# Performance work log

Hardware: AMD Instinct MI355X
Metric: run time of the kernel (lower is better)

## Reference

```python
import jax, jax.numpy as jnp
import numpy as np

D = 1024
H = 16
DK = D // H
E = 8
DFF = 4 * D
TOPK = 2
EPS = 1e-5


def setup_inputs() -> dict:
    key = jax.random.key(0)
    ks = jax.random.split(key, 16)
    s_in = 1.0 / np.sqrt(D)
    s_ff = 1.0 / np.sqrt(DFF)
    return {
        "x": jax.random.normal(ks[0], (2, 2048, D), dtype=jnp.float32),
        "ln1_g": jnp.ones((D,), jnp.float32),
        "ln1_b": jnp.zeros((D,), jnp.float32),
        "w_qkv": jax.random.normal(ks[1], (D, 3 * D), jnp.float32) * s_in,
        "b_qkv": jnp.zeros((3 * D,), jnp.float32),
        "w_o": jax.random.normal(ks[2], (D, D), jnp.float32) * s_in,
        "b_o": jnp.zeros((D,), jnp.float32),
        "ln2_g": jnp.ones((D,), jnp.float32),
        "ln2_b": jnp.zeros((D,), jnp.float32),
        "gate_w": jax.random.normal(ks[3], (D, E), jnp.float32) * s_in,
        "gate_b": jnp.zeros((E,), jnp.float32),
        "W1": jax.random.normal(ks[4], (E, D, DFF), jnp.float32) * s_in,
        "b1": jnp.zeros((E, DFF), jnp.float32),
        "W2": jax.random.normal(ks[5], (E, DFF, D), jnp.float32) * s_ff,
        "b2": jnp.zeros((E, D), jnp.float32),
    }


def _layernorm(x, g, b):
    m = jnp.mean(x, axis=-1, keepdims=True)
    v = jnp.mean(jnp.square(x - m), axis=-1, keepdims=True)
    return (x - m) * jax.lax.rsqrt(v + EPS) * g + b


def reference(x, ln1_g, ln1_b, w_qkv, b_qkv, w_o, b_o, ln2_g, ln2_b,
              gate_w, gate_b, W1, b1, W2, b2):
    B, S, _ = x.shape
    # --- attention (pre-LN, residual) ---
    h = _layernorm(x, ln1_g, ln1_b)
    qkv = h @ w_qkv + b_qkv                      # [B,S,3D]
    q, k, v = jnp.split(qkv, 3, axis=-1)
    q = q.reshape(B, S, H, DK)
    k = k.reshape(B, S, H, DK)
    v = v.reshape(B, S, H, DK)
    scores = jnp.einsum('bqhd,bkhd->bhqk', q, k) / np.sqrt(DK)
    attn = jax.nn.softmax(scores, axis=-1)
    o = jnp.einsum('bhqk,bkhd->bqhd', attn, v).reshape(B, S, D)
    x = x + o @ w_o + b_o
    # --- MoE (pre-LN, residual) ---
    h = _layernorm(x, ln2_g, ln2_b).reshape(B * S, D)   # [T,D]
    logits = h @ gate_w + gate_b                        # [T,E]
    topv, topi = jax.lax.top_k(logits, TOPK)            # [T,K]
    gw = jax.nn.softmax(topv, axis=-1)                  # [T,K]
    # per-token per-expert combine weight (0 if expert not selected)
    ew = jnp.sum(jax.nn.one_hot(topi, E, dtype=h.dtype) * gw[..., None], axis=1)  # [T,E]
    hid = jax.nn.relu(jnp.einsum('td,edf->etf', h, W1) + b1[:, None, :])  # [E,T,DFF]
    out_e = jnp.einsum('etf,efd->etd', hid, W2) + b2[:, None, :]          # [E,T,D]
    moe = jnp.einsum('etd,te->td', out_e, ew)
    return x + moe.reshape(B, S, D)
```

## Files before the change

kernel.cpp:

```cpp
#include <hip/hip_runtime.h>

#define TT 4096
#define SS 2048
#define DD 1024
#define NH 16
#define NE 8
#define DFFC 4096

typedef _Float16 h8  __attribute__((ext_vector_type(8)));
typedef _Float16 h4v __attribute__((ext_vector_type(4)));
typedef float    f4  __attribute__((ext_vector_type(4)));

typedef __attribute__((address_space(3))) void lds_void;
typedef __attribute__((address_space(1))) const void gbl_void;

__device__ __forceinline__ f4 mfma16(h8 a, h8 b, f4 c){
  return __builtin_amdgcn_mfma_f32_16x16x32_f16(a, b, c, 0, 0, 0);
}
__device__ __forceinline__ void fsplit(float x, _Float16& hi, _Float16& lo){
  _Float16 h = (_Float16)x; hi = h; lo = (_Float16)(x - (float)h);
}
__device__ __forceinline__ void gll16(const void* g, void* l){
  __builtin_amdgcn_global_load_lds((gbl_void*)g, (lds_void*)l, 16, 0, 0);
}

template<int SPLIT>
__global__ __launch_bounds__(256) void conv_t(
    const float* __restrict__ in, _Float16* __restrict__ oh, _Float16* __restrict__ ol,
    int K, int N)
{
  __shared__ float tile[64][65];
  const int n0 = blockIdx.x*64, k0 = blockIdx.y*64;
  const int tid = threadIdx.x;
  const float* inp = in + (size_t)blockIdx.z*K*N;
  #pragma unroll
  for (int p=0;p<4;++p){
    int row = p*16 + (tid>>4), col4 = (tid&15)*4;
    *(f4*)&tile[row][col4] = *(const f4*)(inp + (size_t)(k0+row)*N + n0 + col4);
  }
  __syncthreads();
  const size_t ob = (size_t)blockIdx.z*K*N;
  #pragma unroll
  for (int p=0;p<2;++p){
    int n = p*32 + (tid>>3), k8 = (tid&7)*8;
    h8 vh, vl;
    #pragma unroll
    for (int j=0;j<8;++j){
      float v = tile[k8+j][n];
      if constexpr (SPLIT){ _Float16 hi,lo; fsplit(v,hi,lo); vh[j]=hi; vl[j]=lo; }
      else vh[j] = (_Float16)v;
    }
    size_t o = ob + (size_t)(n0+n)*K + k0 + k8;
    *(h8*)(oh + o) = vh;
    if constexpr (SPLIT) *(h8*)(ol + o) = vl;
  }
}

template<int MODE>
__global__ __launch_bounds__(256) void ln_kernel(
    const float* __restrict__ in, const float* __restrict__ g, const float* __restrict__ b,
    _Float16* __restrict__ outHi, _Float16* __restrict__ outLo)
{
  const int t = blockIdx.x, tid = threadIdx.x;
  f4 v = ((const f4*)(in + (size_t)t*DD))[tid];
  float s = v.x+v.y+v.z+v.w;
  float q = v.x*v.x+v.y*v.y+v.z*v.z+v.w*v.w;
  #pragma unroll
  for (int off=32; off; off>>=1){ s += __shfl_xor(s,off); q += __shfl_xor(q,off); }
  __shared__ float red[8];
  int wid = tid>>6, lane = tid&63;
  if (lane==0){ red[wid]=s; red[4+wid]=q; }
  __syncthreads();
  s = red[0]+red[1]+red[2]+red[3];
  q = red[4]+red[5]+red[6]+red[7];
  float mean = s * (1.0f/DD);
  float var  = q * (1.0f/DD) - mean*mean;
  float vv = var + 1e-5f;
  float r = rsqrtf(vv);
  r = r * (1.5f - 0.5f*vv*r*r);
  f4 gv = ((const f4*)g)[tid], bv = ((const f4*)b)[tid];
  #pragma unroll
  for (int j=0;j<4;++j){
    float y = (v[j]-mean)*r*gv[j] + bv[j];
    size_t o = (size_t)t*DD + tid*4 + j;
    if constexpr (MODE==0){ _Float16 hi,lo; fsplit(y,hi,lo); outHi[o]=hi; outLo[o]=lo; }
    else { outHi[o]=(_Float16)y; }
  }
}

template<int MODE>
__global__ __launch_bounds__(256,2) void gemm_split3(
    const _Float16* __restrict__ Ah, const _Float16* __restrict__ Al,
    const _Float16* __restrict__ Bh, const _Float16* __restrict__ Bl,
    const float* __restrict__ bias,
    _Float16* __restrict__ Chi, _Float16* __restrict__ Clo,
    float* __restrict__ Cf, const float* __restrict__ resid,
    int N, int K, int GM)
{
  __shared__ __align__(16) char smem[65536];
  const int tid = threadIdx.x, lane = tid&63, wid = tid>>6;
  const int l15 = lane&15, l4 = lane>>4;
  const int bid = blockIdx.x;
  const int c = bid & 7, rr = bid >> 3, mpx = GM >> 3;
  const int tm = (c*mpx + (rr % mpx))*128, tn = (rr / mpx)*128;

  const _Float16* sA[4]; const _Float16* sB[4];
  #pragma unroll
  for (int i=0;i<4;++i){
    int row = i*32 + (tid>>3);
    int s = (tid&7) ^ (row&7);
    int plane = s>>2, koff = (s&3)*8;
    sA[i] = (plane ? Al : Ah) + (size_t)(tm+row)*K + koff;
    sB[i] = (plane ? Bl : Bh) + (size_t)(tn+row)*K + koff;
  }
  int offAh[4], offAl[4], offBh[4], offBl[4];
  #pragma unroll
  for (int m=0;m<4;++m){
    int rowA = (wid>>1)*64 + m*16 + l15;
    offAh[m] = rowA*64 + ((l4 ^ (rowA&7))<<3);
    offAl[m] = rowA*64 + (((4|l4) ^ (rowA&7))<<3);
    int rowB = (wid&1)*64 + m*16 + l15;
    offBh[m] = rowB*64 + ((l4 ^ (rowB&7))<<3);
    offBl[m] = rowB*64 + (((4|l4) ^ (rowB&7))<<3);
  }
  #pragma unroll
  for (int i=0;i<4;++i){
    int L = i*4096 + tid*16;
    gll16(sA[i], smem + L);
    gll16(sB[i], smem + 16384 + L);
  }
  __syncthreads();
  f4 acc[4][4] = {};
  int cur = 0;
  for (int k0=0; k0<K; k0+=32){
    if (k0+32 < K){
      int nb = (cur^1)*32768;
      #pragma unroll
      for (int i=0;i<4;++i){
        int L = i*4096 + tid*16;
        gll16(sA[i]+k0+32, smem + nb + L);
        gll16(sB[i]+k0+32, smem + nb + 16384 + L);
      }
    }
    const _Float16* As = (const _Float16*)(smem + cur*32768);
    const _Float16* Bs = (const _Float16*)(smem + cur*32768 + 16384);
    h8 ah[4], al[4], bh4[4], bl4[4];
    #pragma unroll
    for (int m=0;m<4;++m){ ah[m] = *(const h8*)&As[offAh[m]]; al[m] = *(const h8*)&As[offAl[m]]; }
    #pragma unroll
    for (int n=0;n<4;++n){ bh4[n] = *(const h8*)&Bs[offBh[n]]; bl4[n] = *(const h8*)&Bs[offBl[n]]; }
    #pragma unroll
    for (int n=0;n<4;++n)
      #pragma unroll
      for (int m=0;m<4;++m){
        acc[m][n] = mfma16(ah[m], bh4[n], acc[m][n]);
        acc[m][n] = mfma16(ah[m], bl4[n], acc[m][n]);
        acc[m][n] = mfma16(al[m], bh4[n], acc[m][n]);
      }
    __syncthreads();
    cur ^= 1;
  }
  const int wm = (wid>>1)*64, wn = (wid&1)*64;
  #pragma unroll
  for (int n=0;n<4;++n){
    int col = tn + wn + n*16 + l15;
    float bv = bias[col];
    #pragma unroll
    for (int m=0;m<4;++m)
      #pragma unroll
      for (int r=0;r<4;++r){
        int rowg = tm + wm + m*16 + l4*4 + r;
        float vv = acc[m][n][r] + bv;
        size_t co = (size_t)rowg*N + col;
        if constexpr (MODE==0){ _Float16 hi,lo; fsplit(vv,hi,lo); Chi[co]=hi; Clo[co]=lo; }
        else { Cf[co] = vv + resid[co]; }
      }
  }
}

__global__ __launch_bounds__(256) void vt_kernel(
    const _Float16* __restrict__ qkvH, const _Float16* __restrict__ qkvL,
    _Float16* __restrict__ vtH, _Float16* __restrict__ vtL)
{
  __shared__ _Float16 TH[64*72], TL[64*72];
  const int tid = threadIdx.x;
  const int tt = blockIdx.x*64;
  const int bh = blockIdx.y;
  const int b = bh>>4, h = bh&15;
  const size_t t0 = (size_t)b*SS;
  #pragma unroll
  for (int p=0;p<2;++p){
    int t = p*32 + (tid>>3), d0 = (tid&7)*8;
    size_t g = (t0 + tt + t)*(size_t)3072 + 2048 + h*64 + d0;
    h8 vh = *(const h8*)(qkvH+g), vl = *(const h8*)(qkvL+g);
    int cp = ((t>>3) ^ (tid&7)) & 7;
    int base = cp*8 + (t&7);
    #pragma unroll
    for (int j=0;j<8;++j){ TH[(d0+j)*72 + base] = vh[j]; TL[(d0+j)*72 + base] = vl[j]; }
  }
  __syncthreads();
  int d = tid>>2, seg = tid&3;
  size_t ob = ((size_t)bh*64 + d)*2048 + tt;
  #pragma unroll
  for (int jj=0;jj<2;++jj){
    int cch = jj*4 + seg, cp = (cch ^ (d>>3)) & 7;
    h8 vh = *(const h8*)&TH[d*72 + cp*8];
    h8 vl = *(const h8*)&TL[d*72 + cp*8];
    *(h8*)(vtH + ob + cch*8) = vh;
    *(h8*)(vtL + ob + cch*8) = vl;
  }
}

__global__ __launch_bounds__(256,3) void attn_kernel(
    const _Float16* __restrict__ qkvH, const _Float16* __restrict__ qkvL,
    const _Float16* __restrict__ vtH, const _Float16* __restrict__ vtL,
    _Float16* __restrict__ oH, _Float16* __restrict__ oL)
{
  __shared__ __align__(16) _Float16 KsH[64*64], KsL[64*64], VsH[64*64], VsL[64*64];
  __shared__ __align__(16) _Float16 Plds[8192];
  const int tid = threadIdx.x, lane = tid & 63, wid = tid >> 6;
  const int l15 = lane & 15, l4 = lane >> 4;
  const int qt = blockIdx.x, bh = blockIdx.y;
  const int b = bh >> 4, h = bh & 15;
  const size_t t0 = (size_t)b * SS;
  const int qbase = qt*128 + wid*32;

  const int srow = tid>>3;
  const int ss = (tid&7) ^ (srow&7);
  const _Float16* kH = qkvH + (t0 + srow)*(size_t)3072 + 1024 + h*64 + ss*8;
  const _Float16* kL = qkvL + (t0 + srow)*(size_t)3072 + 1024 + h*64 + ss*8;
  const _Float16* vH = vtH + ((size_t)bh*64 + srow)*2048 + ss*8;
  const _Float16* vL = vtL + ((size_t)bh*64 + srow)*2048 + ss*8;
  const int ldsL0 = tid*16;

  int offF[4][2];
  #pragma unroll
  for (int n=0;n<4;++n)
    #pragma unroll
    for (int ks=0;ks<2;++ks){
      int row = n*16 + l15;
      offF[n][ks] = row*64 + (((ks*4 + l4) ^ (row&7))<<3);
    }
  int pq[2], psw[2], prb[2];
  #pragma unroll
  for (int m=0;m<2;++m){
    int q = m*16 + l15;
    pq[m]  = wid*4096 + q*64;
    psw[m] = (q&3)<<4;
    prb[m] = pq[m] + ((l4*16) ^ psw[m]);
  }

  h8 qh[2][2], ql[2][2];
  #pragma unroll
  for (int m=0;m<2;++m)
    #pragma unroll
    for (int ks=0;ks<2;++ks){
      size_t go = (t0 + qbase + m*16 + l15)*(size_t)3072 + h*64 + ks*32 + l4*8;
      qh[m][ks] = *(const h8*)(qkvH + go);
      ql[m][ks] = *(const h8*)(qkvL + go);
    }

  f4 oacc[2][4] = {};
  float psum[2] = {0.f, 0.f};

  for (int kv=0; kv<SS; kv+=64){
    #pragma unroll
    for (int cc=0; cc<2; ++cc){
      size_t kgo = (size_t)(kv + cc*32)*3072;
      size_t vgo = (size_t)kv + (size_t)cc*32*2048;
      int L = cc*4096 + ldsL0;
      gll16(kH + kgo, (char*)KsH + L);
      gll16(kL + kgo, (char*)KsL + L);
      gll16(vH + vgo, (char*)VsH + L);
      gll16(vL + vgo, (char*)VsL + L);
    }
    __syncthreads();

    #pragma unroll
    for (int half=0; half<2; ++half){
      f4 s[2][2] = {};
      __builtin_amdgcn_s_setprio(1);
      #pragma unroll
      for (int n2=0;n2<2;++n2){
        int nn = half*2 + n2;
        #pragma unroll
        for (int ks=0;ks<2;++ks){
          h8 kh = *(const h8*)&KsH[offF[nn][ks]];
          h8 kl = *(const h8*)&KsL[offF[nn][ks]];
          s[0][n2] = mfma16(kh, qh[0][ks], s[0][n2]);
          s[0][n2] = mfma16(kl, qh[0][ks], s[0][n2]);
          s[0][n2] = mfma16(kh, ql[0][ks], s[0][n2]);
          s[1][n2] = mfma16(kh, qh[1][ks], s[1][n2]);
          s[1][n2] = mfma16(kl, qh[1][ks], s[1][n2]);
          s[1][n2] = mfma16(kh, ql[1][ks], s[1][n2]);
        }
      }
      __builtin_amdgcn_s_setprio(0);
      #pragma unroll
      for (int m=0;m<2;++m){
        #pragma unroll
        for (int n2=0;n2<2;++n2){
          f4 sv = s[m][n2];
          float p0 = __expf(fmaf(sv.x, 0.125f, -8.0f));
          float p1 = __expf(fmaf(sv.y, 0.125f, -8.0f));
          float p2 = __expf(fmaf(sv.z, 0.125f, -8.0f));
          float p3 = __expf(fmaf(sv.w, 0.125f, -8.0f));
          psum[m] += (p0+p1)+(p2+p3);
          h4v hv, lv; _Float16 hh, ll;
          fsplit(p0,hh,ll); hv[0]=hh; lv[0]=ll;
          fsplit(p1,hh,ll); hv[1]=hh; lv[1]=ll;
          fsplit(p2,hh,ll); hv[2]=hh; lv[2]=ll;
          fsplit(p3,hh,ll); hv[3]=hh; lv[3]=ll;
          int wb = pq[m] + ((n2*32 + l4*8) ^ psw[m]);
          *(h4v*)((char*)Plds + wb) = hv;
          *(h4v*)((char*)Plds + 2048 + wb) = lv;
        }
      }
      __builtin_amdgcn_s_setprio(1);
      h8 paH0 = *(const h8*)((char*)Plds + prb[0]);
      h8 paL0 = *(const h8*)((char*)Plds + 2048 + prb[0]);
      h8 paH1 = *(const h8*)((char*)Plds + prb[1]);
      h8 paL1 = *(const h8*)((char*)Plds + 2048 + prb[1]);
      #pragma unroll
      for (int nd=0;nd<4;++nd){
        h8 vh = *(const h8*)&VsH[offF[nd][half]];
        h8 vl = *(const h8*)&VsL[offF[nd][half]];
        oacc[0][nd] = mfma16(paH0, vh, oacc[0][nd]);
        oacc[0][nd] = mfma16(paH0, vl, oacc[0][nd]);
        oacc[0][nd] = mfma16(paL0, vh, oacc[0][nd]);
        oacc[1][nd] = mfma16(paH1, vh, oacc[1][nd]);
        oacc[1][nd] = mfma16(paH1, vl, oacc[1][nd]);
        oacc[1][nd] = mfma16(paL1, vh, oacc[1][nd]);
      }
      __builtin_amdgcn_s_setprio(0);
    }
    __syncthreads();
  }

  #pragma unroll
  for (int m=0;m<2;++m){
    float ls = psum[m];
    ls += __shfl_xor(ls, 16);
    ls += __shfl_xor(ls, 32);
    #pragma unroll
    for (int r=0;r<4;++r){
      int srcl = l4*4 + r;
      float lq = __uint_as_float(
          (unsigned)__builtin_amdgcn_ds_bpermute(srcl*4, (int)__float_as_uint(ls)));
      float linv = 1.0f / lq;
      #pragma unroll
      for (int nd=0;nd<4;++nd){
        float vv = oacc[m][nd][r] * linv;
        size_t go = (t0 + qbase + m*16 + l4*4 + r)*(size_t)DD + h*64 + nd*16 + l15;
        _Float16 hi, lo; fsplit(vv, hi, lo);
        oH[go] = hi; oL[go] = lo;
      }
    }
  }
}

__global__ __launch_bounds__(64) void gate_kernel(
    const float* __restrict__ x1, const float* __restrict__ g, const float* __restrict__ bb,
    const float* __restrict__ gw, const float* __restrict__ gb,
    int* __restrict__ topi, float* __restrict__ topw, int* __restrict__ cnt)
{
  const int t = blockIdx.x, lane = threadIdx.x;
  f4 xv[4];
  float s=0.f, q=0.f;
  #pragma unroll
  for (int i=0;i<4;++i){
    xv[i] = ((const f4*)(x1 + (size_t)t*DD))[lane + i*64];
    #pragma unroll
    for (int j=0;j<4;++j){ s += xv[i][j]; q += xv[i][j]*xv[i][j]; }
  }
  #pragma unroll
  for (int off=32; off; off>>=1){ s += __shfl_xor(s,off); q += __shfl_xor(q,off); }
  float mean = s*(1.f/DD), var = q*(1.f/DD)-mean*mean, vv = var+1e-5f;
  float r = rsqrtf(vv); r = r*(1.5f-0.5f*vv*r*r);
  float acc[8] = {0,0,0,0,0,0,0,0};
  #pragma unroll
  for (int i=0;i<4;++i){
    f4 gv = ((const f4*)g)[lane+i*64], bv = ((const f4*)bb)[lane+i*64];
    #pragma unroll
    for (int j=0;j<4;++j){
      int d = (lane+i*64)*4 + j;
      float hv = (xv[i][j]-mean)*r*gv[j] + bv[j];
      const f4* gp = (const f4*)(gw + (size_t)d*8);
      f4 g0 = gp[0], g1 = gp[1];
      acc[0]+=hv*g0.x; acc[1]+=hv*g0.y; acc[2]+=hv*g0.z; acc[3]+=hv*g0.w;
      acc[4]+=hv*g1.x; acc[5]+=hv*g1.y; acc[6]+=hv*g1.z; acc[7]+=hv*g1.w;
    }
  }
  #pragma unroll
  for (int e=0;e<8;++e)
    #pragma unroll
    for (int off=32;off;off>>=1) acc[e]+=__shfl_xor(acc[e],off);
  if (lane==0){
    float lg[8];
    #pragma unroll
    for (int e=0;e<8;++e) lg[e]=acc[e]+gb[e];
    int i0=0; float v0=lg[0];
    #pragma unroll
    for (int e=1;e<8;++e) if (lg[e]>v0){ v0=lg[e]; i0=e; }
    int i1=-1; float v1=-1e30f;
    #pragma unroll
    for (int e=0;e<8;++e) if (e!=i0 && lg[e]>v1){ v1=lg[e]; i1=e; }
    float w0 = 1.f/(1.f+__expf(v1-v0));
    topi[2*t]=i0; topi[2*t+1]=i1;
    topw[2*t]=w0; topw[2*t+1]=1.f-w0;
    atomicAdd(&cnt[i0],1); atomicAdd(&cnt[i1],1);
  }
}

__global__ void scan_kernel(const int* __restrict__ cnt, int* __restrict__ offs,
                            int* __restrict__ cursor, int* __restrict__ pref1,
                            int* __restrict__ pref2){
  if (threadIdx.x==0){
    int s=0, t1=0, t2=0;
    for (int e=0;e<8;++e){
      offs[e]=s; s+=cnt[e];
      int mt = (cnt[e]+127)>>7;
      pref1[e]=t1; t1 += mt*(DFFC/128);
      pref2[e]=t2; t2 += mt*(DD/128);
    }
    offs[8]=s; pref1[8]=t1; pref2[8]=t2;
  }
  if (threadIdx.x<8) cursor[threadIdx.x]=0;
}

__global__ __launch_bounds__(256) void scatter_kernel(
    const int* __restrict__ topi, const int* __restrict__ offs, int* __restrict__ cursor,
    int* __restrict__ tokl, int* __restrict__ posof)
{
  int t = blockIdx.x*256 + threadIdx.x;
  #pragma unroll
  for (int k=0;k<2;++k){
    int e = topi[2*t+k];
    int p = atomicAdd(&cursor[e],1);
    int idx = offs[e]+p;
    tokl[idx]=t; posof[2*t+k]=idx;
  }
}

template<int GATHER>
__global__ __launch_bounds__(256,2) void gemm_ffn(
    const _Float16* __restrict__ A, const _Float16* __restrict__ Bw,
    const float* __restrict__ bias, _Float16* __restrict__ C,
    const int* __restrict__ tok, const int* __restrict__ offs,
    const int* __restrict__ pref, int N, int K)
{
  __shared__ __align__(16) char smem[65536];
  const int tid = threadIdx.x, lane = tid&63, wid = tid>>6;
  const int l15 = lane&15, l4 = lane>>4;
  const int wm = (wid>>1)*64, wn = (wid&1)*64;
  const int tot = pref[8];

  int offA[4][2], offB[4][2];
  #pragma unroll
  for (int m=0;m<4;++m)
    #pragma unroll
    for (int ks=0;ks<2;++ks){
      int rowA = wm + m*16 + l15;
      offA[m][ks] = rowA*64 + (((ks*4+l4) ^ (rowA&7))<<3);
      int rowB = wn + m*16 + l15;
      offB[m][ks] = rowB*64 + (((ks*4+l4) ^ (rowB&7))<<3);
    }

  for (int idx = blockIdx.x; idx < tot; idx += gridDim.x){
    int e = 0;
    #pragma unroll
    for (int k=1;k<8;++k) if (pref[k] <= idx) e = k;
    const int off = offs[e], Me = offs[e+1]-off;
    const int mt = (Me+127)>>7;
    const int local = idx - pref[e];
    const int ni = local / mt, mi = local - ni*mt;
    const int tm = mi*128, tn = ni*128;
    const _Float16* Bp = Bw + (size_t)e*N*K + (size_t)tn*K;
    const float* biasp = bias + (size_t)e*N;

    const _Float16* sA[4]; const _Float16* sB[4];
    #pragma unroll
    for (int i=0;i<4;++i){
      int row = i*32 + (tid>>3);
      int s = (tid&7) ^ (row&7);
      int lr = min(tm+row, Me-1);
      size_t ar = GATHER ? (size_t)tok[off+lr] : (size_t)(off+lr);
      sA[i] = A + ar*K + s*8;
      sB[i] = Bp + (size_t)row*K + s*8;
    }
    #pragma unroll
    for (int i=0;i<4;++i){
      int L = i*4096 + tid*16;
      gll16(sA[i], smem + L);
      gll16(sB[i], smem + 16384 + L);
    }
    __syncthreads();
    f4 acc[4][4] = {};
    int cur = 0;
    for (int k0=0; k0<K; k0+=64){
      if (k0+64 < K){
        int nb = (cur^1)*32768;
        #pragma unroll
        for (int i=0;i<4;++i){
          int L = i*4096 + tid*16;
          gll16(sA[i]+k0+64, smem + nb + L);
          gll16(sB[i]+k0+64, smem + nb + 16384 + L);
        }
      }
      const _Float16* As = (const _Float16*)(smem + cur*32768);
      const _Float16* Bs = (const _Float16*)(smem + cur*32768 + 16384);
      #pragma unroll
      for (int ks=0;ks<2;++ks){
        h8 av[4], bv[4];
        #pragma unroll
        for (int m=0;m<4;++m) av[m] = *(const h8*)&As[offA[m][ks]];
        #pragma unroll
        for (int n=0;n<4;++n) bv[n] = *(const h8*)&Bs[offB[n][ks]];
        #pragma unroll
        for (int n=0;n<4;++n)
          #pragma unroll
          for (int m=0;m<4;++m)
            acc[m][n] = mfma16(av[m], bv[n], acc[m][n]);
      }
      __syncthreads();
      cur ^= 1;
    }
    _Float16* Cs = (_Float16*)smem;
    float bvv[4];
    #pragma unroll
    for (int n=0;n<4;++n) bvv[n] = biasp[tn + wn + n*16 + l15];
    #pragma unroll
    for (int p=0;p<2;++p){
      if ((wid&1)==p){
        #pragma unroll
        for (int n=0;n<4;++n)
          #pragma unroll
          for (int m=0;m<4;++m)
            #pragma unroll
            for (int r=0;r<4;++r){
              int row = wm + m*16 + l4*4 + r;
              float vv = acc[m][n][r] + bvv[n];
              if constexpr (GATHER) vv = fmaxf(vv, 0.f);
              Cs[row*72 + n*16 + l15] = (_Float16)vv;
            }
      }
      __syncthreads();
      int row = tid>>1, seg = tid&1;
      if (tm+row < Me){
        size_t gb = (size_t)(off+tm+row)*N + tn + p*64 + seg*32;
        #pragma unroll
        for (int j=0;j<4;++j)
          *(h8*)(C + gb + j*8) = *(const h8*)&Cs[row*72 + seg*32 + j*8];
      }
      __syncthreads();
    }
  }
}

__global__ __launch_bounds__(256) void combine_kernel(
    const float* __restrict__ x1, const _Float16* __restrict__ moe,
    const float* __restrict__ topw, const int* __restrict__ posof, float* __restrict__ out)
{
  int t = blockIdx.x, tid = threadIdx.x;
  size_t o = (size_t)t*DD + tid*4;
  f4 xv = *(const f4*)(x1+o);
  int p0=posof[2*t], p1=posof[2*t+1];
  float w0=topw[2*t], w1=topw[2*t+1];
  h4v m0 = *(const h4v*)(moe + (size_t)p0*DD + tid*4);
  h4v m1 = *(const h4v*)(moe + (size_t)p1*DD + tid*4);
  f4 r;
  #pragma unroll
  for (int j=0;j<4;++j) r[j] = xv[j] + w0*(float)m0[j] + w1*(float)m1[j];
  *(f4*)(out+o) = r;
}

extern "C" void kernel_launch(void* const* d_in, const int* in_sizes, int n_in,
                              void* d_out, int out_size, void* d_ws, size_t ws_size,
                              hipStream_t stream)
{
  (void)in_sizes; (void)n_in; (void)out_size; (void)ws_size;
  const float* x     = (const float*)d_in[0];
  const float* ln1g  = (const float*)d_in[1];
  const float* ln1b  = (const float*)d_in[2];
  const float* wqkv  = (const float*)d_in[3];
  const float* bqkv  = (const float*)d_in[4];
  const float* wo    = (const float*)d_in[5];
  const float* bo    = (const float*)d_in[6];
  const float* ln2g  = (const float*)d_in[7];
  const float* ln2b  = (const float*)d_in[8];
  const float* gatew = (const float*)d_in[9];
  const float* gateb = (const float*)d_in[10];
  const float* W1    = (const float*)d_in[11];
  const float* b1    = (const float*)d_in[12];
  const float* W2    = (const float*)d_in[13];
  const float* b2    = (const float*)d_in[14];
  float* out = (float*)d_out;

  char* w = (char*)d_ws;
  _Float16* W1T    = (_Float16*)(w);
  _Float16* W2T    = (_Float16*)(w + 67108864);
  _Float16* wqT_H  = (_Float16*)(w + 134217728);
  _Float16* wqT_L  = (_Float16*)(w + 140509184);
  _Float16* woT_H  = (_Float16*)(w + 146800640);
  _Float16* woT_L  = (_Float16*)(w + 148897792);
  char* rb = w + 150994944;
  _Float16* h1H  = (_Float16*)(rb);
  _Float16* h1L  = (_Float16*)(rb + 8388608);
  _Float16* vtH  = (_Float16*)(rb);
  _Float16* vtL  = (_Float16*)(rb + 8388608);
  _Float16* qkvH = (_Float16*)(rb + 16777216);
  _Float16* qkvL = (_Float16*)(rb + 41943040);
  _Float16* hid  = (_Float16*)(rb);
  char* rm = w + 218103808;
  _Float16* oH  = (_Float16*)(rm);
  _Float16* oL  = (_Float16*)(rm + 8388608);
  _Float16* moe = (_Float16*)(rm);
  float* x1     = (float*)(w + 234881024);
  _Float16* h2h = (_Float16*)(w + 251658240);
  char* sm = w + 260046848;
  float* topw  = (float*)(sm);
  int*   topi  = (int*)(sm + 32768);
  int*   posof = (int*)(sm + 65536);
  int*   tokl  = (int*)(sm + 98304);
  int*   cnt   = (int*)(sm + 131072);
  int*   offs  = (int*)(sm + 131072 + 64);
  int*   cursor= (int*)(sm + 131072 + 128);
  int*   pref1 = (int*)(sm + 131072 + 192);
  int*   pref2 = (int*)(sm + 131072 + 256);

  conv_t<1><<<dim3(48, 16, 1), 256, 0, stream>>>(wqkv, wqT_H, wqT_L, 1024, 3072);
  conv_t<1><<<dim3(16, 16, 1), 256, 0, stream>>>(wo,   woT_H, woT_L, 1024, 1024);
  conv_t<0><<<dim3(64, 16, 8), 256, 0, stream>>>(W1, W1T, nullptr, 1024, 4096);
  conv_t<0><<<dim3(16, 64, 8), 256, 0, stream>>>(W2, W2T, nullptr, 4096, 1024);

  ln_kernel<0><<<TT, 256, 0, stream>>>(x, ln1g, ln1b, h1H, h1L);
  gemm_split3<0><<<768, 256, 0, stream>>>(
      h1H, h1L, wqT_H, wqT_L, bqkv, qkvH, qkvL, nullptr, nullptr, 3072, 1024, 32);
  vt_kernel<<<dim3(32, 32), 256, 0, stream>>>(qkvH, qkvL, vtH, vtL);
  attn_kernel<<<dim3(SS/128, 2*NH), 256, 0, stream>>>(qkvH, qkvL, vtH, vtL, oH, oL);
  gemm_split3<1><<<256, 256, 0, stream>>>(
      oH, oL, woT_H, woT_L, bo, nullptr, nullptr, x1, x, 1024, 1024, 32);
  ln_kernel<1><<<TT, 256, 0, stream>>>(x1, ln2g, ln2b, h2h, nullptr);
  hipMemsetAsync(cnt, 0, 8*sizeof(int), stream);
  gate_kernel<<<TT, 64, 0, stream>>>(x1, ln2g, ln2b, gatew, gateb, topi, topw, cnt);
  scan_kernel<<<1, 32, 0, stream>>>(cnt, offs, cursor, pref1, pref2);
  scatter_kernel<<<TT/256, 256, 0, stream>>>(topi, offs, cursor, tokl, posof);
  gemm_ffn<1><<<512, 256, 0, stream>>>(h2h, W1T, b1, hid, tokl, offs, pref1, DFFC, 1024);
  gemm_ffn<0><<<512, 256, 0, stream>>>(hid, W2T, b2, moe, tokl, offs, pref2, DD, DFFC);
  combine_kernel<<<TT, 256, 0, stream>>>(x1, moe, topw, posof, out);
}
```

Measured before the change: 793.1 us.

## Single-buffer LDS in GEMMs, split-K the second FFN GEMM, swizzle blocks

Both GEMM kernels drop LDS double buffering, halving shared memory to 32 KB, and raise their launch bounds to get more resident blocks per CU. The down-projection FFN GEMM is split into two K halves written to separate fp16 buffers, which the combine kernel sums, so there are more tiles to spread over the grid. FFN grids double to 1024 blocks and use an XCD-aware block swizzle. The cost is that global loads no longer overlap MFMA work inside a block, there is an extra partial-sum buffer to read and write, and the halves are rounded to fp16 separately before summing.

```diff
diff --git a/kernel.cpp b/kernel.cpp
--- a/kernel.cpp
+++ b/kernel.cpp
@@ -89,7 +89,7 @@
 }
 
 template<int MODE>
-__global__ __launch_bounds__(256,2) void gemm_split3(
+__global__ __launch_bounds__(256,3) void gemm_split3(
     const _Float16* __restrict__ Ah, const _Float16* __restrict__ Al,
     const _Float16* __restrict__ Bh, const _Float16* __restrict__ Bl,
     const float* __restrict__ bias,
@@ -97,7 +97,7 @@
     float* __restrict__ Cf, const float* __restrict__ resid,
     int N, int K, int GM)
 {
-  __shared__ __align__(16) char smem[65536];
+  __shared__ __align__(16) char smem[32768];
   const int tid = threadIdx.x, lane = tid&63, wid = tid>>6;
   const int l15 = lane&15, l4 = lane>>4;
   const int bid = blockIdx.x;
@@ -123,27 +123,17 @@
     offBh[m] = rowB*64 + ((l4 ^ (rowB&7))<<3);
     offBl[m] = rowB*64 + (((4|l4) ^ (rowB&7))<<3);
   }
-  #pragma unroll
-  for (int i=0;i<4;++i){
-    int L = i*4096 + tid*16;
-    gll16(sA[i], smem + L);
-    gll16(sB[i], smem + 16384 + L);
-  }
-  __syncthreads();
   f4 acc[4][4] = {};
-  int cur = 0;
+  const _Float16* As = (const _Float16*)(smem);
+  const _Float16* Bs = (const _Float16*)(smem + 16384);
   for (int k0=0; k0<K; k0+=32){
-    if (k0+32 < K){
-      int nb = (cur^1)*32768;
-      #pragma unroll
-      for (int i=0;i<4;++i){
-        int L = i*4096 + tid*16;
-        gll16(sA[i]+k0+32, smem + nb + L);
-        gll16(sB[i]+k0+32, smem + nb + 16384 + L);
-      }
-    }
-    const _Float16* As = (const _Float16*)(smem + cur*32768);
-    const _Float16* Bs = (const _Float16*)(smem + cur*32768 + 16384);
+    #pragma unroll
+    for (int i=0;i<4;++i){
+      int L = i*4096 + tid*16;
+      gll16(sA[i]+k0, smem + L);
+      gll16(sB[i]+k0, smem + 16384 + L);
+    }
+    __syncthreads();
     h8 ah[4], al[4], bh4[4], bl4[4];
     #pragma unroll
     for (int m=0;m<4;++m){ ah[m] = *(const h8*)&As[offAh[m]]; al[m] = *(const h8*)&As[offAl[m]]; }
@@ -158,7 +148,6 @@
         acc[m][n] = mfma16(al[m], bh4[n], acc[m][n]);
       }
     __syncthreads();
-    cur ^= 1;
   }
   const int wm = (wid>>1)*64, wn = (wid&1)*64;
   #pragma unroll
@@ -421,7 +410,7 @@
       offs[e]=s; s+=cnt[e];
       int mt = (cnt[e]+127)>>7;
       pref1[e]=t1; t1 += mt*(DFFC/128);
-      pref2[e]=t2; t2 += mt*(DD/128);
+      pref2[e]=t2; t2 += mt*(DD/128)*2;
     }
     offs[8]=s; pref1[8]=t1; pref2[8]=t2;
   }
@@ -442,18 +431,20 @@
   }
 }
 
-template<int GATHER>
-__global__ __launch_bounds__(256,2) void gemm_ffn(
+template<int GATHER, int KH>
+__global__ __launch_bounds__(256,4) void gemm_ffn(
     const _Float16* __restrict__ A, const _Float16* __restrict__ Bw,
-    const float* __restrict__ bias, _Float16* __restrict__ C,
+    const float* __restrict__ bias, _Float16* __restrict__ C0, _Float16* __restrict__ C1,
     const int* __restrict__ tok, const int* __restrict__ offs,
     const int* __restrict__ pref, int N, int K)
 {
-  __shared__ __align__(16) char smem[65536];
+  __shared__ __align__(16) char smem[32768];
   const int tid = threadIdx.x, lane = tid&63, wid = tid>>6;
   const int l15 = lane&15, l4 = lane>>4;
   const int wm = (wid>>1)*64, wn = (wid&1)*64;
   const int tot = pref[8];
+  const int nt = N>>7;
+  const int KSEG = K/KH;
 
   int offA[4][2], offB[4][2];
   #pragma unroll
@@ -466,15 +457,20 @@
       offB[m][ks] = rowB*64 + (((ks*4+l4) ^ (rowB&7))<<3);
     }
 
-  for (int idx = blockIdx.x; idx < tot; idx += gridDim.x){
+  const int cpx = gridDim.x >> 3;
+  const int bswz = (blockIdx.x & 7)*cpx + (blockIdx.x >> 3);
+  for (int idx = bswz; idx < tot; idx += gridDim.x){
     int e = 0;
     #pragma unroll
     for (int k=1;k<8;++k) if (pref[k] <= idx) e = k;
     const int off = offs[e], Me = offs[e+1]-off;
     const int mt = (Me+127)>>7;
-    const int local = idx - pref[e];
+    int local = idx - pref[e];
+    int kh = 0;
+    if constexpr (KH==2){ int per = mt*nt; kh = (local >= per); local -= kh*per; }
     const int ni = local / mt, mi = local - ni*mt;
     const int tm = mi*128, tn = ni*128;
+    const int kb = kh*KSEG;
     const _Float16* Bp = Bw + (size_t)e*N*K + (size_t)tn*K;
     const float* biasp = bias + (size_t)e*N;
 
@@ -485,30 +481,20 @@
       int s = (tid&7) ^ (row&7);
       int lr = min(tm+row, Me-1);
       size_t ar = GATHER ? (size_t)tok[off+lr] : (size_t)(off+lr);
-      sA[i] = A + ar*K + s*8;
-      sB[i] = Bp + (size_t)row*K + s*8;
-    }
-    #pragma unroll
-    for (int i=0;i<4;++i){
-      int L = i*4096 + tid*16;
-      gll16(sA[i], smem + L);
-      gll16(sB[i], smem + 16384 + L);
-    }
-    __syncthreads();
+      sA[i] = A + ar*K + s*8 + kb;
+      sB[i] = Bp + (size_t)row*K + s*8 + kb;
+    }
     f4 acc[4][4] = {};
-    int cur = 0;
-    for (int k0=0; k0<K; k0+=64){
-      if (k0+64 < K){
-        int nb = (cur^1)*32768;
-        #pragma unroll
-        for (int i=0;i<4;++i){
-          int L = i*4096 + tid*16;
-          gll16(sA[i]+k0+64, smem + nb + L);
-          gll16(sB[i]+k0+64, smem + nb + 16384 + L);
-        }
-      }
-      const _Float16* As = (const _Float16*)(smem + cur*32768);
-      const _Float16* Bs = (const _Float16*)(smem + cur*32768 + 16384);
+    const _Float16* As = (const _Float16*)(smem);
+    const _Float16* Bs = (const _Float16*)(smem + 16384);
+    for (int k0=0; k0<KSEG; k0+=64){
+      #pragma unroll
+      for (int i=0;i<4;++i){
+        int L = i*4096 + tid*16;
+        gll16(sA[i]+k0, smem + L);
+        gll16(sB[i]+k0, smem + 16384 + L);
+      }
+      __syncthreads();
       #pragma unroll
       for (int ks=0;ks<2;++ks){
         h8 av[4], bv[4];
@@ -523,12 +509,12 @@
             acc[m][n] = mfma16(av[m], bv[n], acc[m][n]);
       }
       __syncthreads();
-      cur ^= 1;
-    }
+    }
+    _Float16* Cp = (KH==2 && kh==1) ? C1 : C0;
     _Float16* Cs = (_Float16*)smem;
     float bvv[4];
     #pragma unroll
-    for (int n=0;n<4;++n) bvv[n] = biasp[tn + wn + n*16 + l15];
+    for (int n=0;n<4;++n) bvv[n] = (KH==2 && kh==1) ? 0.f : biasp[tn + wn + n*16 + l15];
     #pragma unroll
     for (int p=0;p<2;++p){
       if ((wid&1)==p){
@@ -550,7 +536,7 @@
         size_t gb = (size_t)(off+tm+row)*N + tn + p*64 + seg*32;
         #pragma unroll
         for (int j=0;j<4;++j)
-          *(h8*)(C + gb + j*8) = *(const h8*)&Cs[row*72 + seg*32 + j*8];
+          *(h8*)(Cp + gb + j*8) = *(const h8*)&Cs[row*72 + seg*32 + j*8];
       }
       __syncthreads();
     }
@@ -558,7 +544,8 @@
 }
 
 __global__ __launch_bounds__(256) void combine_kernel(
-    const float* __restrict__ x1, const _Float16* __restrict__ moe,
+    const float* __restrict__ x1, const _Float16* __restrict__ moe0,
+    const _Float16* __restrict__ moe1,
     const float* __restrict__ topw, const int* __restrict__ posof, float* __restrict__ out)
 {
   int t = blockIdx.x, tid = threadIdx.x;
@@ -566,11 +553,14 @@
   f4 xv = *(const f4*)(x1+o);
   int p0=posof[2*t], p1=posof[2*t+1];
   float w0=topw[2*t], w1=topw[2*t+1];
-  h4v m0 = *(const h4v*)(moe + (size_t)p0*DD + tid*4);
-  h4v m1 = *(const h4v*)(moe + (size_t)p1*DD + tid*4);
+  h4v a0 = *(const h4v*)(moe0 + (size_t)p0*DD + tid*4);
+  h4v b0 = *(const h4v*)(moe1 + (size_t)p0*DD + tid*4);
+  h4v a1 = *(const h4v*)(moe0 + (size_t)p1*DD + tid*4);
+  h4v b1 = *(const h4v*)(moe1 + (size_t)p1*DD + tid*4);
   f4 r;
   #pragma unroll
-  for (int j=0;j<4;++j) r[j] = xv[j] + w0*(float)m0[j] + w1*(float)m1[j];
+  for (int j=0;j<4;++j)
+    r[j] = xv[j] + w0*((float)a0[j]+(float)b0[j]) + w1*((float)a1[j]+(float)b1[j]);
   *(f4*)(out+o) = r;
 }
 
@@ -603,6 +593,7 @@
   _Float16* wqT_L  = (_Float16*)(w + 140509184);
   _Float16* woT_H  = (_Float16*)(w + 146800640);
   _Float16* woT_L  = (_Float16*)(w + 148897792);
+  _Float16* moe1   = (_Float16*)(w + 134217728);
   char* rb = w + 150994944;
   _Float16* h1H  = (_Float16*)(rb);
   _Float16* h1L  = (_Float16*)(rb + 8388608);
@@ -612,9 +603,9 @@
   _Float16* qkvL = (_Float16*)(rb + 41943040);
   _Float16* hid  = (_Float16*)(rb);
   char* rm = w + 218103808;
-  _Float16* oH  = (_Float16*)(rm);
-  _Float16* oL  = (_Float16*)(rm + 8388608);
-  _Float16* moe = (_Float16*)(rm);
+  _Float16* oH   = (_Float16*)(rm);
+  _Float16* oL   = (_Float16*)(rm + 8388608);
+  _Float16* moe0 = (_Float16*)(rm);
   float* x1     = (float*)(w + 234881024);
   _Float16* h2h = (_Float16*)(w + 251658240);
   char* sm = w + 260046848;
@@ -645,7 +636,9 @@
   gate_kernel<<<TT, 64, 0, stream>>>(x1, ln2g, ln2b, gatew, gateb, topi, topw, cnt);
   scan_kernel<<<1, 32, 0, stream>>>(cnt, offs, cursor, pref1, pref2);
   scatter_kernel<<<TT/256, 256, 0, stream>>>(topi, offs, cursor, tokl, posof);
-  gemm_ffn<1><<<512, 256, 0, stream>>>(h2h, W1T, b1, hid, tokl, offs, pref1, DFFC, 1024);
-  gemm_ffn<0><<<512, 256, 0, stream>>>(hid, W2T, b2, moe, tokl, offs, pref2, DD, DFFC);
-  combine_kernel<<<TT, 256, 0, stream>>>(x1, moe, topw, posof, out);
-}
+  gemm_ffn<1,1><<<1024, 256, 0, stream>>>(
+      h2h, W1T, b1, hid, hid, tokl, offs, pref1, DFFC, 1024);
+  gemm_ffn<0,2><<<1024, 256, 0, stream>>>(
+      hid, W2T, b2, moe0, moe1, tokl, offs, pref2, DD, DFFC);
+  combine_kernel<<<TT, 256, 0, stream>>>(x1, moe0, moe1, topw, posof, out);
+}
```

Result: faster. 730.7 us (-7.9%).
